# Kernel optimization log

Measured on AMD Instinct MI355X. Metric: run time of the kernel, lower is better.

The kernel has to match this reference:

```python
import jax, jax.numpy as jnp
import numpy as np

H = 16  # num_heads
B, N, M, D = 4, 512, 2048, 1024
FF = 4096  # mlp_ratio * D
LN_EPS = 1e-5


def _ln(x, g, b):
    m = x.mean(-1, keepdims=True)
    v = ((x - m) ** 2).mean(-1, keepdims=True)
    return (x - m) * jax.lax.rsqrt(v + LN_EPS) * g + b


def _attn(q_in, k_in, v_in, wq, bq, wk, bk, wv, bv, wp, bp):
    b, n, d = q_in.shape
    m = k_in.shape[1]
    hd = d // H
    scale = hd ** -0.5
    q = (q_in @ wq + bq).reshape(b, n, H, hd) * scale
    k = (k_in @ wk + bk).reshape(b, m, H, hd)
    v = (v_in @ wv + bv).reshape(b, m, H, hd)
    attn = jax.nn.softmax(jnp.einsum('bnhd,bmhd->bhnm', q, k), axis=-1)
    out = jnp.einsum('bhnm,bmhd->bnhd', attn, v).reshape(b, n, d)
    return out @ wp + bp


def setup_inputs() -> dict:
    key = jax.random.key(0)
    ks = iter(jax.random.split(key, 32))
    rnd = lambda shape: jax.random.normal(next(ks), shape, dtype=jnp.float32)
    w = lambda *shape: rnd(shape) * 0.02
    inp = {
        'state': rnd((B, N, D)),
        'patches': rnd((B, M, D)),
        'patches_pos_embed': rnd((B, M, D)),
        'state_query': rnd((B, N, D)),
    }
    for p in ('ca', 'sa'):
        inp[f'{p}_wq'] = w(D, D); inp[f'{p}_bq'] = jnp.zeros((D,), jnp.float32)
        inp[f'{p}_wk'] = w(D, D); inp[f'{p}_bk'] = jnp.zeros((D,), jnp.float32)
        inp[f'{p}_wv'] = w(D, D); inp[f'{p}_bv'] = jnp.zeros((D,), jnp.float32)
        inp[f'{p}_wp'] = w(D, D); inp[f'{p}_bp'] = jnp.zeros((D,), jnp.float32)
    inp['w1'] = w(D, FF); inp['b1'] = jnp.zeros((FF,), jnp.float32)
    inp['w2'] = w(FF, D); inp['b2'] = jnp.zeros((D,), jnp.float32)
    for i in (1, 2, 3):
        inp[f'n{i}_g'] = jnp.ones((D,), jnp.float32)
        inp[f'n{i}_b'] = jnp.zeros((D,), jnp.float32)
        inp[f'ls{i}'] = jnp.full((D,), 1e-5, jnp.float32)
    return inp


def reference(state, patches, patches_pos_embed, state_query,
              ca_wq, ca_bq, ca_wk, ca_bk, ca_wv, ca_bv, ca_wp, ca_bp,
              sa_wq, sa_bq, sa_wk, sa_bk, sa_wv, sa_bv, sa_wp, sa_bp,
              w1, b1, w2, b2,
              n1_g, n1_b, n2_g, n2_b, n3_g, n3_b,
              ls1, ls2, ls3):
    # pre-norm path of TransformerLayer.forward_pre (dropouts/drop_path = 0)
    state = state + state_query
    kv = patches + patches_pos_embed
    cross = _attn(_ln(state, n1_g, n1_b), kv, patches,
                  ca_wq, ca_bq, ca_wk, ca_bk, ca_wv, ca_bv, ca_wp, ca_bp)
    state = state + cross * ls1
    ns = _ln(state, n2_g, n2_b)
    selfa = _attn(ns, ns, ns,
                  sa_wq, sa_bq, sa_wk, sa_bk, sa_wv, sa_bv, sa_wp, sa_bp)
    state = state + selfa * ls2
    h = jax.nn.gelu(_ln(state, n3_g, n3_b) @ w1 + b1)
    return state + (h @ w2 + b2) * ls3
```

## Files before the change

kernel.cpp:

```cpp
#include <hip/hip_runtime.h>

#define DEV __device__ __forceinline__

typedef __bf16 bf16x8 __attribute__((ext_vector_type(8)));
typedef float f32x4 __attribute__((ext_vector_type(4)));

DEV unsigned short f2bf(float f) {
  union { float f; unsigned int u; } v; v.f = f;
  unsigned int r = v.u + 0x7fffu + ((v.u >> 16) & 1u);
  return (unsigned short)(r >> 16);
}
DEV unsigned int pack2(float a, float b) {
  return (unsigned int)f2bf(a) | ((unsigned int)f2bf(b) << 16);
}

DEV void gload16(const void* g, void* l) {
  __builtin_amdgcn_global_load_lds(
      (const __attribute__((address_space(1))) unsigned int*)g,
      (__attribute__((address_space(3))) unsigned int*)l, 16, 0, 0);
}

DEV void tconv_body(const float* __restrict__ W, unsigned short* __restrict__ Wt,
                    int K, int N, int bx, int by) {
  __shared__ float tile[32][33];
  const int tx = threadIdx.x, ty = threadIdx.y;
  const int n0 = bx * 32, k0 = by * 32;
#pragma unroll
  for (int i = 0; i < 32; i += 8)
    tile[ty + i][tx] = W[(size_t)(k0 + ty + i) * N + n0 + tx];
  __syncthreads();
#pragma unroll
  for (int i = 0; i < 32; i += 8)
    Wt[(size_t)(n0 + ty + i) * K + k0 + tx] = f2bf(tile[tx][ty + i]);
}

__global__ __launch_bounds__(256) void tconv_kernel(
    const float* __restrict__ W, unsigned short* __restrict__ Wt, int K, int N) {
  tconv_body(W, Wt, K, N, blockIdx.x, blockIdx.y);
}

struct TC8 { const float* src[8]; unsigned short* dst[8]; };
__global__ __launch_bounds__(256) void tconv8_kernel(TC8 p) {
  tconv_body(p.src[blockIdx.z], p.dst[blockIdx.z], 1024, 1024, blockIdx.x, blockIdx.y);
}

__global__ __launch_bounds__(256) void cat3_kernel(
    const float* __restrict__ a, const float* __restrict__ b,
    const float* __restrict__ c, float* __restrict__ o) {
  const int i = blockIdx.x * 256 + threadIdx.x;
  o[i] = i < 1024 ? a[i] : (i < 2048 ? b[i - 1024] : c[i - 2048]);
}

__global__ __launch_bounds__(256) void vtrans_kernel(
    const unsigned short* __restrict__ V, unsigned short* __restrict__ vT,
    int Nk, int RS, int colbase) {
  __shared__ unsigned short tile[32][33];
  const int tx = threadIdx.x, ty = threadIdx.y;
  const int k0 = blockIdx.x * 32;
  const int h = blockIdx.y >> 1, dt = (blockIdx.y & 1) * 32;
  const int b = blockIdx.z;
#pragma unroll
  for (int i = 0; i < 32; i += 8)
    tile[ty + i][tx] = V[(size_t)(b * Nk + k0 + ty + i) * RS + colbase + h * 64 + dt + tx];
  __syncthreads();
#pragma unroll
  for (int i = 0; i < 32; i += 8)
    vT[((size_t)(b * 16 + h) * 64 + dt + ty + i) * Nk + k0 + tx] = tile[tx][ty + i];
}

__global__ __launch_bounds__(256) void add_ln_kernel(
    const float* __restrict__ a, const float* b, float* x0_out,
    unsigned short* __restrict__ y, const float* __restrict__ gam,
    const float* __restrict__ bet) {
  const int row = blockIdx.x, t = threadIdx.x;
  const int c = t * 4;
  const size_t base = (size_t)row * 1024 + c;
  float4 v = *reinterpret_cast<const float4*>(a + base);
  if (b) {
    float4 v2 = *reinterpret_cast<const float4*>(b + base);
    v.x += v2.x; v.y += v2.y; v.z += v2.z; v.w += v2.w;
  }
  if (x0_out) *reinterpret_cast<float4*>(x0_out + base) = v;
  float s = v.x + v.y + v.z + v.w;
  float sq = v.x * v.x + v.y * v.y + v.z * v.z + v.w * v.w;
#pragma unroll
  for (int o = 32; o > 0; o >>= 1) {
    s += __shfl_xor(s, o);
    sq += __shfl_xor(sq, o);
  }
  __shared__ float ps[4], pq[4];
  const int w = t >> 6;
  if ((t & 63) == 0) { ps[w] = s; pq[w] = sq; }
  __syncthreads();
  s = ps[0] + ps[1] + ps[2] + ps[3];
  sq = pq[0] + pq[1] + pq[2] + pq[3];
  const float mean = s * (1.f / 1024.f);
  const float var = sq * (1.f / 1024.f) - mean * mean;
  const float rstd = rsqrtf(var + 1e-5f);
  float4 gv = *reinterpret_cast<const float4*>(gam + c);
  float4 bv = *reinterpret_cast<const float4*>(bet + c);
  uint2 o2;
  o2.x = pack2((v.x - mean) * rstd * gv.x + bv.x, (v.y - mean) * rstd * gv.y + bv.y);
  o2.y = pack2((v.z - mean) * rstd * gv.z + bv.z, (v.w - mean) * rstd * gv.w + bv.w);
  *reinterpret_cast<uint2*>(y + base) = o2;
}

__global__ __launch_bounds__(256) void kvcast_kernel(
    const float* __restrict__ p, const float* __restrict__ pe,
    unsigned short* __restrict__ kvo, unsigned short* __restrict__ po) {
  const size_t i = ((size_t)blockIdx.x * 256 + threadIdx.x) * 4;
  float4 a = *reinterpret_cast<const float4*>(p + i);
  float4 b = *reinterpret_cast<const float4*>(pe + i);
  uint2 kv2, p2;
  kv2.x = pack2(a.x + b.x, a.y + b.y);
  kv2.y = pack2(a.z + b.z, a.w + b.w);
  p2.x = pack2(a.x, a.y);
  p2.y = pack2(a.z, a.w);
  *reinterpret_cast<uint2*>(kvo + i) = kv2;
  *reinterpret_cast<uint2*>(po + i) = p2;
}

template <int EPI, int BM, int BN>
__global__ __launch_bounds__(256) void gemm_kernel(
    const unsigned short* __restrict__ A, const unsigned short* __restrict__ Bt,
    const float* __restrict__ bias, const float* resid,
    const float* __restrict__ ls, void* outp, int M, int N, int K, int lda) {
  constexpr int WM = BM / 32;
  constexpr int WN = BN / 32;
  __shared__ __align__(16) unsigned short As[2][BM * 32];
  __shared__ __align__(16) unsigned short Bs[2][BN * 32];
  const int t = threadIdx.x;
  const int lane = t & 63, w = t >> 6;
  const int wr = w >> 1, wc = w & 1;
  const int g = lane >> 4, lr = lane & 15;
  const int srow = lane >> 2, scol = (lane & 3) * 8;

  const int gx = gridDim.x, gy = gridDim.y;
  const int gxy = gx * gy;
  const int nwg = gxy * gridDim.z;
  const int orig = (blockIdx.z * gy + blockIdx.y) * gx + blockIdx.x;
  const int q = nwg >> 3, r = nwg & 7;
  const int xcd = orig & 7;
  int wgid = (xcd < r ? xcd * (q + 1) : r * (q + 1) + (xcd - r) * q) + (orig >> 3);
  const int bz = wgid / gxy;
  wgid -= bz * gxy;
  int bx, by;
  if (gy >= gx) { by = wgid / gx; bx = wgid - by * gx; }
  else          { bx = wgid / gy; by = wgid - bx * gy; }
  const int brow = by * BM, bcol = bx * BN;
  const int koff = bz * K;

  f32x4 acc[WM][WN] = {};

  auto stage = [&](int buf, int k0) {
#pragma unroll
    for (int i = 0; i < BM / 64; i++) {
      const int r0 = (i * 4 + w) * 16;
      gload16(A + (size_t)(brow + r0 + srow) * lda + koff + k0 + scol, &As[buf][r0 * 32]);
    }
#pragma unroll
    for (int i = 0; i < BN / 64; i++) {
      const int r0 = (i * 4 + w) * 16;
      gload16(Bt + (size_t)(bcol + r0 + srow) * lda + koff + k0 + scol, &Bs[buf][r0 * 32]);
    }
  };

  stage(0, 0);
  const int nk = K / 32;
  int cur = 0;
  for (int kt = 0; kt < nk; kt++) {
    __syncthreads();
    if (kt + 1 < nk) stage(cur ^ 1, (kt + 1) * 32);
    bf16x8 af[WM], bfr[WN];
#pragma unroll
    for (int m = 0; m < WM; m++)
      af[m] = *reinterpret_cast<const bf16x8*>(
          &As[cur][(wr * (BM / 2) + m * 16 + lr) * 32 + g * 8]);
#pragma unroll
    for (int n = 0; n < WN; n++)
      bfr[n] = *reinterpret_cast<const bf16x8*>(
          &Bs[cur][(wc * (BN / 2) + n * 16 + lr) * 32 + g * 8]);
#pragma unroll
    for (int m = 0; m < WM; m++)
#pragma unroll
      for (int n = 0; n < WN; n++)
        acc[m][n] = __builtin_amdgcn_mfma_f32_16x16x32_bf16(af[m], bfr[n], acc[m][n], 0, 0, 0);
    cur ^= 1;
  }

#pragma unroll
  for (int m = 0; m < WM; m++) {
    const int row0 = brow + wr * (BM / 2) + m * 16 + g * 4;
#pragma unroll
    for (int n = 0; n < WN; n++) {
      const int col = bcol + wc * (BN / 2) + n * 16 + lr;
      const float bv = (EPI == 4) ? 0.f : bias[col];
#pragma unroll
      for (int r = 0; r < 4; r++) {
        const float v = acc[m][n][r] + bv;
        const size_t idx = (size_t)(row0 + r) * N + col;
        if (EPI == 0) {
          ((unsigned short*)outp)[idx] = f2bf(v);
        } else if (EPI == 2) {
          ((float*)outp)[idx] = resid[idx] + v * ls[col];
        } else if (EPI == 3) {
          const float tth = tanhf(0.7978845608028654f * (v + 0.044715f * v * v * v));
          ((unsigned short*)outp)[idx] = f2bf(0.5f * v * (1.f + tth));
        } else {
          ((float*)outp)[(size_t)bz * M * N + idx] = v;
        }
      }
    }
  }
}

__global__ __launch_bounds__(256) void splitk_red_kernel(
    const float* __restrict__ p, const float* __restrict__ bias,
    const float* __restrict__ resid, const float* __restrict__ ls,
    float* __restrict__ out) {
  const size_t i = ((size_t)blockIdx.x * 256 + threadIdx.x) * 4;
  const int c = (int)(i & 1023);
  float4 a = *reinterpret_cast<const float4*>(p + i);
  float4 b = *reinterpret_cast<const float4*>(p + 2048ull * 1024 + i);
  float4 rv = *reinterpret_cast<const float4*>(resid + i);
  float4 bb = *reinterpret_cast<const float4*>(bias + c);
  float4 lv = *reinterpret_cast<const float4*>(ls + c);
  float4 o;
  o.x = rv.x + (a.x + b.x + bb.x) * lv.x;
  o.y = rv.y + (a.y + b.y + bb.y) * lv.y;
  o.z = rv.z + (a.z + b.z + bb.z) * lv.z;
  o.w = rv.w + (a.w + b.w + bb.w) * lv.w;
  *reinterpret_cast<float4*>(out + i) = o;
}

__global__ __launch_bounds__(256) void attn_kernel(
    const unsigned short* __restrict__ Q, const unsigned short* __restrict__ Kp,
    const unsigned short* __restrict__ vT, unsigned short* __restrict__ O,
    int RSq, int RSk, int Nq, int Nk, float scale) {
  __shared__ __align__(16) unsigned short Qs[64 * 72];
  __shared__ __align__(16) unsigned short Ks[2][64 * 72];
  __shared__ __align__(16) unsigned short Vs[2][64 * 72];
  __shared__ __align__(16) unsigned short Ps[64 * 72];
  const int t = threadIdx.x, lane = t & 63, w = t >> 6;
  const int qt = blockIdx.x, h = blockIdx.y, b = blockIdx.z;
  const int g = lane >> 4, lr = lane & 15;
  const int srow = t >> 2, scol = (t & 3) * 16;

  {
    const uint4* gq = reinterpret_cast<const uint4*>(
        Q + (size_t)(b * Nq + qt * 64 + srow) * RSq + h * 64 + scol);
    *reinterpret_cast<uint4*>(&Qs[srow * 72 + scol]) = gq[0];
    *reinterpret_cast<uint4*>(&Qs[srow * 72 + scol + 8]) = gq[1];
  }
  float m_i = -1e30f, l_i = 0.f;
  f32x4 acc_o[4] = {};

  auto kaddr = [&](int kv0) {
    return reinterpret_cast<const uint4*>(
        Kp + (size_t)(b * Nk + kv0 + srow) * RSk + h * 64 + scol);
  };
  auto vaddr = [&](int kv0) {
    return reinterpret_cast<const uint4*>(
        vT + ((size_t)(b * 16 + h) * 64 + srow) * Nk + kv0 + scol);
  };

  uint4 kr0 = kaddr(0)[0], kr1 = kaddr(0)[1];
  uint4 vr0 = vaddr(0)[0], vr1 = vaddr(0)[1];

  int cur = 0;
  for (int kv0 = 0; kv0 < Nk; kv0 += 64) {
    *reinterpret_cast<uint4*>(&Ks[cur][srow * 72 + scol]) = kr0;
    *reinterpret_cast<uint4*>(&Ks[cur][srow * 72 + scol + 8]) = kr1;
    *reinterpret_cast<uint4*>(&Vs[cur][srow * 72 + scol]) = vr0;
    *reinterpret_cast<uint4*>(&Vs[cur][srow * 72 + scol + 8]) = vr1;
    __syncthreads();
    if (kv0 + 64 < Nk) {
      kr0 = kaddr(kv0 + 64)[0]; kr1 = kaddr(kv0 + 64)[1];
      vr0 = vaddr(kv0 + 64)[0]; vr1 = vaddr(kv0 + 64)[1];
    }

    f32x4 accs[4] = {};
    __builtin_amdgcn_s_setprio(1);
#pragma unroll
    for (int d0 = 0; d0 < 64; d0 += 32) {
      bf16x8 qf = *reinterpret_cast<const bf16x8*>(&Qs[(w * 16 + lr) * 72 + d0 + g * 8]);
#pragma unroll
      for (int m = 0; m < 4; m++) {
        bf16x8 kf = *reinterpret_cast<const bf16x8*>(&Ks[cur][(m * 16 + lr) * 72 + d0 + g * 8]);
        accs[m] = __builtin_amdgcn_mfma_f32_16x16x32_bf16(kf, qf, accs[m], 0, 0, 0);
      }
    }
    __builtin_amdgcn_s_setprio(0);
    float pmax = -1e30f;
#pragma unroll
    for (int m = 0; m < 4; m++)
#pragma unroll
      for (int r = 0; r < 4; r++) pmax = fmaxf(pmax, accs[m][r]);
    pmax = fmaxf(pmax, __shfl_xor(pmax, 16));
    pmax = fmaxf(pmax, __shfl_xor(pmax, 32));
    const float m_new = fmaxf(m_i, pmax * scale);
    const float corr = __expf(m_i - m_new);
    float psum = 0.f;
#pragma unroll
    for (int m = 0; m < 4; m++) {
      float p0 = __expf(fmaf(accs[m][0], scale, -m_new));
      float p1 = __expf(fmaf(accs[m][1], scale, -m_new));
      float p2 = __expf(fmaf(accs[m][2], scale, -m_new));
      float p3 = __expf(fmaf(accs[m][3], scale, -m_new));
      psum += p0 + p1 + p2 + p3;
      uint2 pk;
      pk.x = pack2(p0, p1);
      pk.y = pack2(p2, p3);
      *reinterpret_cast<uint2*>(&Ps[(w * 16 + lr) * 72 + m * 16 + g * 4]) = pk;
    }
    psum += __shfl_xor(psum, 16);
    psum += __shfl_xor(psum, 32);
    l_i = l_i * corr + psum;
    m_i = m_new;
#pragma unroll
    for (int r = 0; r < 4; r++) {
      const float cf = __shfl(corr, g * 4 + r);
#pragma unroll
      for (int n = 0; n < 4; n++) acc_o[n][r] *= cf;
    }
    __builtin_amdgcn_s_setprio(1);
#pragma unroll
    for (int ks = 0; ks < 2; ks++) {
      bf16x8 pf = *reinterpret_cast<const bf16x8*>(&Ps[(w * 16 + lr) * 72 + ks * 32 + g * 8]);
#pragma unroll
      for (int n = 0; n < 4; n++) {
        bf16x8 vf = *reinterpret_cast<const bf16x8*>(&Vs[cur][(n * 16 + lr) * 72 + ks * 32 + g * 8]);
        acc_o[n] = __builtin_amdgcn_mfma_f32_16x16x32_bf16(pf, vf, acc_o[n], 0, 0, 0);
      }
    }
    __builtin_amdgcn_s_setprio(0);
    cur ^= 1;
  }
#pragma unroll
  for (int r = 0; r < 4; r++) {
    const float li = __shfl(l_i, g * 4 + r);
    const float inv = 1.f / li;
    const int qrow = qt * 64 + w * 16 + g * 4 + r;
#pragma unroll
    for (int n = 0; n < 4; n++)
      O[(size_t)(b * Nq + qrow) * 1024 + h * 64 + n * 16 + lr] = f2bf(acc_o[n][r] * inv);
  }
}

extern "C" void kernel_launch(void* const* d_in, const int* in_sizes, int n_in,
                              void* d_out, int out_size, void* d_ws, size_t ws_size,
                              hipStream_t stream) {
  const float* state = (const float*)d_in[0];
  const float* patches = (const float*)d_in[1];
  const float* ppe = (const float*)d_in[2];
  const float* squery = (const float*)d_in[3];
  const float* ca_wq = (const float*)d_in[4];
  const float* ca_bq = (const float*)d_in[5];
  const float* ca_wk = (const float*)d_in[6];
  const float* ca_bk = (const float*)d_in[7];
  const float* ca_wv = (const float*)d_in[8];
  const float* ca_bv = (const float*)d_in[9];
  const float* ca_wp = (const float*)d_in[10];
  const float* ca_bp = (const float*)d_in[11];
  const float* sa_wq = (const float*)d_in[12];
  const float* sa_bq = (const float*)d_in[13];
  const float* sa_wk = (const float*)d_in[14];
  const float* sa_bk = (const float*)d_in[15];
  const float* sa_wv = (const float*)d_in[16];
  const float* sa_bv = (const float*)d_in[17];
  const float* sa_wp = (const float*)d_in[18];
  const float* sa_bp = (const float*)d_in[19];
  const float* w1 = (const float*)d_in[20];
  const float* b1 = (const float*)d_in[21];
  const float* w2 = (const float*)d_in[22];
  const float* b2 = (const float*)d_in[23];
  const float* n1_g = (const float*)d_in[24];
  const float* n1_b = (const float*)d_in[25];
  const float* ls1 = (const float*)d_in[26];
  const float* n2_g = (const float*)d_in[27];
  const float* n2_b = (const float*)d_in[28];
  const float* ls2 = (const float*)d_in[29];
  const float* n3_g = (const float*)d_in[30];
  const float* n3_b = (const float*)d_in[31];
  const float* ls3 = (const float*)d_in[32];

  char* wsp = (char*)d_ws;
  auto alloc = [&](size_t bytes) {
    void* p = (void*)wsp;
    wsp += (bytes + 255) & ~(size_t)255;
    return p;
  };
  float* stateF = (float*)alloc(2048ull * 1024 * 4);
  unsigned short* lnB = (unsigned short*)alloc(2048ull * 1024 * 2);
  unsigned short* kvB = (unsigned short*)alloc(8192ull * 1024 * 2);
  unsigned short* patB = (unsigned short*)alloc(8192ull * 1024 * 2);
  unsigned short* qB = (unsigned short*)alloc(2048ull * 1024 * 2);
  unsigned short* kB = (unsigned short*)alloc(8192ull * 1024 * 2);
  unsigned short* vB = (unsigned short*)alloc(8192ull * 1024 * 2);
  unsigned short* oB = (unsigned short*)alloc(2048ull * 1024 * 2);
  unsigned short* hB = kvB;
  unsigned short* qkvB = kB;
  unsigned short* vTc = patB;
  unsigned short* vTs = qB;
  float* mlp2p = (float*)patB;
  unsigned short* ca_wqt = (unsigned short*)alloc(1024ull * 1024 * 2);
  unsigned short* ca_wkt = (unsigned short*)alloc(1024ull * 1024 * 2);
  unsigned short* ca_wvt = (unsigned short*)alloc(1024ull * 1024 * 2);
  unsigned short* ca_wpt = (unsigned short*)alloc(1024ull * 1024 * 2);
  unsigned short* sa_wqkvt = (unsigned short*)alloc(3072ull * 1024 * 2);
  unsigned short* sa_wpt = (unsigned short*)alloc(1024ull * 1024 * 2);
  unsigned short* w1t = (unsigned short*)alloc(4096ull * 1024 * 2);
  unsigned short* w2t = (unsigned short*)alloc(4096ull * 1024 * 2);
  float* sa_bqkv = (float*)alloc(3072 * 4);

  const dim3 tb(32, 8);
  TC8 tc;
  tc.src[0] = ca_wq; tc.dst[0] = ca_wqt;
  tc.src[1] = ca_wk; tc.dst[1] = ca_wkt;
  tc.src[2] = ca_wv; tc.dst[2] = ca_wvt;
  tc.src[3] = ca_wp; tc.dst[3] = ca_wpt;
  tc.src[4] = sa_wq; tc.dst[4] = sa_wqkvt;
  tc.src[5] = sa_wk; tc.dst[5] = sa_wqkvt + 1024ull * 1024;
  tc.src[6] = sa_wv; tc.dst[6] = sa_wqkvt + 2048ull * 1024;
  tc.src[7] = sa_wp; tc.dst[7] = sa_wpt;
  tconv8_kernel<<<dim3(32, 32, 8), tb, 0, stream>>>(tc);
  tconv_kernel<<<dim3(128, 32), tb, 0, stream>>>(w1, w1t, 1024, 4096);
  tconv_kernel<<<dim3(32, 128), tb, 0, stream>>>(w2, w2t, 4096, 1024);
  cat3_kernel<<<12, 256, 0, stream>>>(sa_bq, sa_bk, sa_bv, sa_bqkv);

  add_ln_kernel<<<2048, 256, 0, stream>>>(state, squery, stateF, lnB, n1_g, n1_b);
  kvcast_kernel<<<8192, 256, 0, stream>>>(patches, ppe, kvB, patB);

  const float qscale = 0.125f;
  gemm_kernel<0, 64, 64><<<dim3(16, 32), 256, 0, stream>>>(lnB, ca_wqt, ca_bq, nullptr, nullptr, qB, 2048, 1024, 1024, 1024);
  gemm_kernel<0, 128, 64><<<dim3(16, 64), 256, 0, stream>>>(kvB, ca_wkt, ca_bk, nullptr, nullptr, kB, 8192, 1024, 1024, 1024);
  gemm_kernel<0, 128, 64><<<dim3(16, 64), 256, 0, stream>>>(patB, ca_wvt, ca_bv, nullptr, nullptr, vB, 8192, 1024, 1024, 1024);
  vtrans_kernel<<<dim3(64, 32, 4), tb, 0, stream>>>(vB, vTc, 2048, 1024, 0);
  attn_kernel<<<dim3(8, 16, 4), 256, 0, stream>>>(qB, kB, vTc, oB, 1024, 1024, 512, 2048, qscale);
  gemm_kernel<2, 64, 64><<<dim3(16, 32), 256, 0, stream>>>(oB, ca_wpt, ca_bp, stateF, ls1, stateF, 2048, 1024, 1024, 1024);

  add_ln_kernel<<<2048, 256, 0, stream>>>(stateF, nullptr, nullptr, lnB, n2_g, n2_b);
  gemm_kernel<0, 128, 64><<<dim3(48, 16), 256, 0, stream>>>(lnB, sa_wqkvt, sa_bqkv, nullptr, nullptr, qkvB, 2048, 3072, 1024, 1024);
  vtrans_kernel<<<dim3(16, 32, 4), tb, 0, stream>>>(qkvB, vTs, 512, 3072, 2048);
  attn_kernel<<<dim3(8, 16, 4), 256, 0, stream>>>(qkvB, qkvB + 1024, vTs, oB, 3072, 3072, 512, 512, qscale);
  gemm_kernel<2, 64, 64><<<dim3(16, 32), 256, 0, stream>>>(oB, sa_wpt, sa_bp, stateF, ls2, stateF, 2048, 1024, 1024, 1024);

  add_ln_kernel<<<2048, 256, 0, stream>>>(stateF, nullptr, nullptr, lnB, n3_g, n3_b);
  gemm_kernel<3, 128, 64><<<dim3(64, 16), 256, 0, stream>>>(lnB, w1t, b1, nullptr, nullptr, hB, 2048, 4096, 1024, 1024);
  gemm_kernel<4, 64, 64><<<dim3(16, 32, 2), 256, 0, stream>>>(hB, w2t, nullptr, nullptr, nullptr, mlp2p, 2048, 1024, 2048, 4096);
  splitk_red_kernel<<<2048, 256, 0, stream>>>(mlp2p, b2, stateF, ls3, (float*)d_out);
}
```

Before: 338.8 us.

## Use exp2 softmax with lazy rescale, hardware bf16 packing, and regridded attention

```diff
diff --git a/kernel.cpp b/kernel.cpp
--- a/kernel.cpp
+++ b/kernel.cpp
@@ -6,12 +6,13 @@
 typedef float f32x4 __attribute__((ext_vector_type(4)));
 
 DEV unsigned short f2bf(float f) {
-  union { float f; unsigned int u; } v; v.f = f;
-  unsigned int r = v.u + 0x7fffu + ((v.u >> 16) & 1u);
-  return (unsigned short)(r >> 16);
-}
-DEV unsigned int pack2(float a, float b) {
-  return (unsigned int)f2bf(a) | ((unsigned int)f2bf(b) << 16);
+  __bf16 h = (__bf16)f;
+  return __builtin_bit_cast(unsigned short, h);
+}
+DEV unsigned int cvtpk(float lo, float hi) {
+  unsigned int r;
+  asm("v_cvt_pk_bf16_f32 %0, %1, %2" : "=v"(r) : "v"(lo), "v"(hi));
+  return r;
 }
 
 DEV void gload16(const void* g, void* l) {
@@ -100,8 +101,8 @@
   float4 gv = *reinterpret_cast<const float4*>(gam + c);
   float4 bv = *reinterpret_cast<const float4*>(bet + c);
   uint2 o2;
-  o2.x = pack2((v.x - mean) * rstd * gv.x + bv.x, (v.y - mean) * rstd * gv.y + bv.y);
-  o2.y = pack2((v.z - mean) * rstd * gv.z + bv.z, (v.w - mean) * rstd * gv.w + bv.w);
+  o2.x = cvtpk((v.x - mean) * rstd * gv.x + bv.x, (v.y - mean) * rstd * gv.y + bv.y);
+  o2.y = cvtpk((v.z - mean) * rstd * gv.z + bv.z, (v.w - mean) * rstd * gv.w + bv.w);
   *reinterpret_cast<uint2*>(y + base) = o2;
 }
 
@@ -112,10 +113,10 @@
   float4 a = *reinterpret_cast<const float4*>(p + i);
   float4 b = *reinterpret_cast<const float4*>(pe + i);
   uint2 kv2, p2;
-  kv2.x = pack2(a.x + b.x, a.y + b.y);
-  kv2.y = pack2(a.z + b.z, a.w + b.w);
-  p2.x = pack2(a.x, a.y);
-  p2.y = pack2(a.z, a.w);
+  kv2.x = cvtpk(a.x + b.x, a.y + b.y);
+  kv2.y = cvtpk(a.z + b.z, a.w + b.w);
+  p2.x = cvtpk(a.x, a.y);
+  p2.y = cvtpk(a.z, a.w);
   *reinterpret_cast<uint2*>(kvo + i) = kv2;
   *reinterpret_cast<uint2*>(po + i) = p2;
 }
@@ -236,13 +237,13 @@
 __global__ __launch_bounds__(256) void attn_kernel(
     const unsigned short* __restrict__ Q, const unsigned short* __restrict__ Kp,
     const unsigned short* __restrict__ vT, unsigned short* __restrict__ O,
-    int RSq, int RSk, int Nq, int Nk, float scale) {
+    int RSq, int RSk, int Nq, int Nk, float k2 ) {
   __shared__ __align__(16) unsigned short Qs[64 * 72];
   __shared__ __align__(16) unsigned short Ks[2][64 * 72];
   __shared__ __align__(16) unsigned short Vs[2][64 * 72];
   __shared__ __align__(16) unsigned short Ps[64 * 72];
   const int t = threadIdx.x, lane = t & 63, w = t >> 6;
-  const int qt = blockIdx.x, h = blockIdx.y, b = blockIdx.z;
+  const int qt = blockIdx.y, h = blockIdx.x & 15, b = blockIdx.x >> 4;
   const int g = lane >> 4, lr = lane & 15;
   const int srow = t >> 2, scol = (t & 3) * 16;
 
@@ -298,31 +299,35 @@
       for (int r = 0; r < 4; r++) pmax = fmaxf(pmax, accs[m][r]);
     pmax = fmaxf(pmax, __shfl_xor(pmax, 16));
     pmax = fmaxf(pmax, __shfl_xor(pmax, 32));
-    const float m_new = fmaxf(m_i, pmax * scale);
-    const float corr = __expf(m_i - m_new);
+    const float pm2 = pmax * k2;
+    if (!__all(pm2 <= m_i + 8.f)) {
+      const float m_new = fmaxf(m_i, pm2);
+      const float corr = exp2f(m_i - m_new);
+      m_i = m_new;
+      l_i *= corr;
+#pragma unroll
+      for (int r = 0; r < 4; r++) {
+        const float cf = __shfl(corr, g * 4 + r);
+#pragma unroll
+        for (int n = 0; n < 4; n++) acc_o[n][r] *= cf;
+      }
+    }
     float psum = 0.f;
 #pragma unroll
     for (int m = 0; m < 4; m++) {
-      float p0 = __expf(fmaf(accs[m][0], scale, -m_new));
-      float p1 = __expf(fmaf(accs[m][1], scale, -m_new));
-      float p2 = __expf(fmaf(accs[m][2], scale, -m_new));
-      float p3 = __expf(fmaf(accs[m][3], scale, -m_new));
+      float p0 = exp2f(fmaf(accs[m][0], k2, -m_i));
+      float p1 = exp2f(fmaf(accs[m][1], k2, -m_i));
+      float p2 = exp2f(fmaf(accs[m][2], k2, -m_i));
+      float p3 = exp2f(fmaf(accs[m][3], k2, -m_i));
       psum += p0 + p1 + p2 + p3;
       uint2 pk;
-      pk.x = pack2(p0, p1);
-      pk.y = pack2(p2, p3);
+      pk.x = cvtpk(p0, p1);
+      pk.y = cvtpk(p2, p3);
       *reinterpret_cast<uint2*>(&Ps[(w * 16 + lr) * 72 + m * 16 + g * 4]) = pk;
     }
     psum += __shfl_xor(psum, 16);
     psum += __shfl_xor(psum, 32);
-    l_i = l_i * corr + psum;
-    m_i = m_new;
-#pragma unroll
-    for (int r = 0; r < 4; r++) {
-      const float cf = __shfl(corr, g * 4 + r);
-#pragma unroll
-      for (int n = 0; n < 4; n++) acc_o[n][r] *= cf;
-    }
+    l_i += psum;
     __builtin_amdgcn_s_setprio(1);
 #pragma unroll
     for (int ks = 0; ks < 2; ks++) {
@@ -431,18 +436,18 @@
   add_ln_kernel<<<2048, 256, 0, stream>>>(state, squery, stateF, lnB, n1_g, n1_b);
   kvcast_kernel<<<8192, 256, 0, stream>>>(patches, ppe, kvB, patB);
 
-  const float qscale = 0.125f;
+  const float k2 = 0.125f * 1.4426950408889634f;
   gemm_kernel<0, 64, 64><<<dim3(16, 32), 256, 0, stream>>>(lnB, ca_wqt, ca_bq, nullptr, nullptr, qB, 2048, 1024, 1024, 1024);
   gemm_kernel<0, 128, 64><<<dim3(16, 64), 256, 0, stream>>>(kvB, ca_wkt, ca_bk, nullptr, nullptr, kB, 8192, 1024, 1024, 1024);
   gemm_kernel<0, 128, 64><<<dim3(16, 64), 256, 0, stream>>>(patB, ca_wvt, ca_bv, nullptr, nullptr, vB, 8192, 1024, 1024, 1024);
   vtrans_kernel<<<dim3(64, 32, 4), tb, 0, stream>>>(vB, vTc, 2048, 1024, 0);
-  attn_kernel<<<dim3(8, 16, 4), 256, 0, stream>>>(qB, kB, vTc, oB, 1024, 1024, 512, 2048, qscale);
+  attn_kernel<<<dim3(64, 8), 256, 0, stream>>>(qB, kB, vTc, oB, 1024, 1024, 512, 2048, k2);
   gemm_kernel<2, 64, 64><<<dim3(16, 32), 256, 0, stream>>>(oB, ca_wpt, ca_bp, stateF, ls1, stateF, 2048, 1024, 1024, 1024);
 
   add_ln_kernel<<<2048, 256, 0, stream>>>(stateF, nullptr, nullptr, lnB, n2_g, n2_b);
   gemm_kernel<0, 128, 64><<<dim3(48, 16), 256, 0, stream>>>(lnB, sa_wqkvt, sa_bqkv, nullptr, nullptr, qkvB, 2048, 3072, 1024, 1024);
   vtrans_kernel<<<dim3(16, 32, 4), tb, 0, stream>>>(qkvB, vTs, 512, 3072, 2048);
-  attn_kernel<<<dim3(8, 16, 4), 256, 0, stream>>>(qkvB, qkvB + 1024, vTs, oB, 3072, 3072, 512, 512, qscale);
+  attn_kernel<<<dim3(64, 8), 256, 0, stream>>>(qkvB, qkvB + 1024, vTs, oB, 3072, 3072, 512, 512, k2);
   gemm_kernel<2, 64, 64><<<dim3(16, 32), 256, 0, stream>>>(oB, sa_wpt, sa_bp, stateF, ls2, stateF, 2048, 1024, 1024, 1024);
 
   add_ln_kernel<<<2048, 256, 0, stream>>>(stateF, nullptr, nullptr, lnB, n3_g, n3_b);
```

Result: no change. 336.8 us (-0.6%).
